# Performance work log

Hardware: AMD Instinct MI355X
Metric: run time of the kernel (lower is better)

## Reference

```python
import jax, jax.numpy as jnp
import numpy as np

N = 16384        # nodes
E = 262144       # edges (avg degree 16)
MUL = 64         # multiplicity per irrep
RDIM = 8         # radial embedding dim
NEURONS = 64     # radial MLP hidden width
NSPECIES = 4
AVG_NEIGH = 16.0
SQRT3 = 1.7320508075688772


def setup_inputs() -> dict:
    key = jax.random.key(0)
    k = jax.random.split(key, 16)
    ey1 = jax.random.normal(k[3], (E, 3), jnp.float32)
    ey1 = ey1 / jnp.linalg.norm(ey1, axis=-1, keepdims=True)  # l=1 spherical harmonics ~ unit edge vectors
    return {
        'node_x0': jax.random.normal(k[0], (N, MUL), jnp.float32),
        'node_x1': jax.random.normal(k[1], (N, MUL, 3), jnp.float32),
        'edge_y0': jnp.ones((E,), jnp.float32),            # l=0 SH is constant
        'edge_y1': ey1,
        'radial_embedding': jax.random.uniform(k[4], (E, RDIM), jnp.float32),
        'senders': jax.random.randint(k[5], (E,), 0, N, dtype=jnp.int32),
        'receivers': jax.random.randint(k[6], (E,), 0, N, dtype=jnp.int32),
        'node_species': jax.random.randint(k[7], (N,), 0, NSPECIES, dtype=jnp.int32),
        'Wup0': jax.random.normal(k[8], (MUL, MUL), jnp.float32),
        'Wup1': jax.random.normal(k[9], (MUL, MUL), jnp.float32),
        'Rw1': jax.random.normal(k[10], (RDIM, NEURONS), jnp.float32),
        'Rw2': jax.random.normal(k[11], (NEURONS, 4 * MUL), jnp.float32),
        'Wd0': jax.random.normal(k[12], (2 * MUL, 2 * MUL), jnp.float32),
        'Wd1': jax.random.normal(k[13], (2 * MUL, MUL), jnp.float32),
        'Wsc0': jax.random.normal(k[14], (NSPECIES, MUL, 2 * MUL), jnp.float32),
        'Wsc1': jax.random.normal(k[15], (NSPECIES, MUL, MUL), jnp.float32),
    }


def reference(node_x0, node_x1, edge_y0, edge_y1, radial_embedding,
              senders, receivers, node_species,
              Wup0, Wup1, Rw1, Rw2, Wd0, Wd1, Wsc0, Wsc1):
    inv = 1.0 / jnp.sqrt(jnp.float32(MUL))
    # ---- linear_up: per-irrep channel mixing --------------------------------
    h0 = (node_x0 @ Wup0) * inv                              # [N, MUL] 0e
    h1 = jnp.einsum('nmc,mk->nkc', node_x1, Wup1) * inv      # [N, MUL, 3] 1o
    # ---- radial MLP -> per-edge tensor-product path weights -----------------
    hid = jax.nn.silu((radial_embedding @ Rw1) / jnp.sqrt(jnp.float32(RDIM)))
    w = ((hid @ Rw2) / jnp.sqrt(jnp.float32(NEURONS))).reshape(E, 4, MUL)
    # ---- gather sender features ---------------------------------------------
    s0 = h0[senders]                                         # [E, MUL]
    s1 = h1[senders]                                         # [E, MUL, 3]
    # ---- CG tensor product (lmax=1) with radial weights ----------------------
    m0a = w[:, 0] * s0 * edge_y0[:, None]                    # 0e x 0e -> 0e
    m0b = w[:, 1] * jnp.einsum('emc,ec->em', s1, edge_y1) / SQRT3  # 1o . 1o -> 0e
    m1a = w[:, 2][:, :, None] * s0[:, :, None] * edge_y1[:, None, :]  # 0e x 1o -> 1o
    m1b = w[:, 3][:, :, None] * s1 * edge_y0[:, None, None]          # 1o x 0e -> 1o
    # ---- scatter-sum to receivers, normalize by sqrt(avg_num_neighbours) ----
    denom = jnp.sqrt(jnp.float32(AVG_NEIGH))
    a0 = jax.ops.segment_sum(jnp.concatenate([m0a, m0b], axis=-1), receivers, num_segments=N) / denom  # [N, 2*MUL]
    a1 = jax.ops.segment_sum(jnp.concatenate([m1a, m1b], axis=1), receivers, num_segments=N) / denom   # [N, 2*MUL, 3]
    # ---- linear_down to gate irreps (MUL scalars + MUL gates, MUL vectors) ---
    inv2 = 1.0 / jnp.sqrt(jnp.float32(2 * MUL))
    d0 = (a0 @ Wd0) * inv2                                   # [N, 2*MUL]
    d1 = jnp.einsum('nmc,mk->nkc', a1, Wd1) * inv2           # [N, MUL, 3]
    # ---- species-indexed self connection (gather weights by species) --------
    all0 = jnp.einsum('nm,smk->nsk', node_x0, Wsc0) * inv    # [N, S, 2*MUL]
    sc0 = jnp.take_along_axis(all0, node_species[:, None, None], axis=1)[:, 0]
    all1 = jnp.einsum('nmc,smk->nskc', node_x1, Wsc1) * inv  # [N, S, MUL, 3]
    sc1 = jnp.take_along_axis(all1, node_species[:, None, None, None], axis=1)[:, 0]
    f0 = 0.5 * (d0 + sc0)
    f1 = 0.5 * (d1 + sc1)
    # ---- equivariant gate: even_act on scalars, even_gate_act on gates ------
    scalars = jax.nn.silu(f0[:, :MUL])                       # [N, MUL]
    gates = jax.nn.silu(f0[:, MUL:])                         # [N, MUL]
    vectors = f1 * gates[:, :, None]                         # [N, MUL, 3]
    return scalars, vectors
```

## Files before the change

kernel.cpp:

```cpp
#include <hip/hip_runtime.h>

#define NN 16384
#define NE 262144
#define N64 (NN * 64)

typedef unsigned short u16;
typedef __attribute__((ext_vector_type(8))) short short8;
typedef __attribute__((ext_vector_type(4))) float f32x4;

__device__ __forceinline__ float us2f(u16 u) {
    union { unsigned int i; float f; } v; v.i = ((unsigned int)u) << 16; return v.f;
}
__device__ __forceinline__ u16 f2us(float x) {
    union { float f; unsigned int i; } u; u.f = x;
    unsigned int r = u.i + 0x7FFF + ((u.i >> 16) & 1);
    return (u16)(r >> 16);
}
__device__ __forceinline__ float silu_f(float x) { return x / (1.0f + __expf(-x)); }
__device__ __forceinline__ float ldf(const void* p, long i, int f) {
    return f ? ((const float*)p)[i] : us2f(((const u16*)p)[i]);
}
__device__ __forceinline__ void ld8(const void* p, long v8, int f, float* o) {
    if (f) {
        const f32x4* q = (const f32x4*)p + v8 * 2;
        f32x4 a = q[0], b = q[1];
        o[0] = a[0]; o[1] = a[1]; o[2] = a[2]; o[3] = a[3];
        o[4] = b[0]; o[5] = b[1]; o[6] = b[2]; o[7] = b[3];
    } else {
        short8 s = ((const short8*)p)[v8];
#pragma unroll
        for (int j = 0; j < 8; j++) o[j] = us2f((u16)s[j]);
    }
}
__device__ __forceinline__ void st8(u16* d, const float* o) {
    short8 s;
#pragma unroll
    for (int j = 0; j < 8; j++) s[j] = (short)f2us(o[j]);
    *reinterpret_cast<short8*>(d) = s;
}
__device__ __forceinline__ short8 f32x8_to_bf16(const float* p) {
    f32x4 a = *reinterpret_cast<const f32x4*>(p);
    f32x4 b = *reinterpret_cast<const f32x4*>(p + 4);
    short8 r;
    r[0] = (short)f2us(a[0]); r[1] = (short)f2us(a[1]);
    r[2] = (short)f2us(a[2]); r[3] = (short)f2us(a[3]);
    r[4] = (short)f2us(b[0]); r[5] = (short)f2us(b[1]);
    r[6] = (short)f2us(b[2]); r[7] = (short)f2us(b[3]);
    return r;
}

__global__ void k_sniff(const u16* __restrict__ re, int* __restrict__ flag,
                        int* __restrict__ cnt) {
    int i = blockIdx.x * 256 + threadIdx.x;
    if (i < NN) cnt[i] = 0;
    if (blockIdx.x == 0 && threadIdx.x < 64) {
        int t = threadIdx.x;
        int hit = (re[t] >= 0x4000) ? 1 : 0;
        unsigned long long b = __ballot(hit);
        if (t == 0) *flag = (__popcll(b) >= 4) ? 1 : 0;
    }
}

#define SB0 1048576L
#define SB1 4194304L
#define SB2 4456448L
#define SB3 5242880L
#define SB4 7340032L
#define SB5 7344128L
#define SB6 7348224L
#define SB7 7348736L
#define SB8 7365120L
#define SB9 7381504L
#define SB10 7389696L
#define SB11 7422464L
#define SB12 7438848L

__global__ void k_convert(const void* x0, const void* x1, const void* ey0, const void* ey1,
                          const void* re, const void* Wup0, const void* Wup1, const void* Rw1,
                          const void* Rw2, const void* Wd0, const void* Wd1, const void* Wsc0,
                          const void* Wsc1, const int* __restrict__ flag,
                          const int* __restrict__ recv, int* __restrict__ cnt,
                          u16* c_x0, u16* x1T, u16* c_ey0, u16* c_ey1, u16* c_re,
                          u16* c_Wup0, u16* c_Wup1, u16* c_Rw1, u16* c_Rw2,
                          u16* c_Wd0, u16* c_Wd1, u16* c_Wsc0, u16* c_Wsc1) {
    long i = (long)blockIdx.x * 256 + threadIdx.x;
    int f = *flag;
    if (i < NE) atomicAdd(&cnt[recv[i]], 1);
    if (i < 131072) {
        float o[8]; ld8(x0, i, f, o); st8(c_x0 + i * 8, o);
    } else if (i < 262144) {
        long v = i - 131072;
        int n = (int)(v >> 3), k8 = (int)(v & 7);
        long b8 = (long)n * 24 + (long)k8 * 3;
        float o[24];
        ld8(x1, b8, f, o); ld8(x1, b8 + 1, f, o + 8); ld8(x1, b8 + 2, f, o + 16);
#pragma unroll
        for (int c = 0; c < 3; c++) {
            float t[8];
#pragma unroll
            for (int k = 0; k < 8; k++) t[k] = o[k * 3 + c];
            st8(x1T + (long)c * N64 + (long)n * 64 + k8 * 8, t);
        }
    } else if (i < 294912) {
        long v = i - 262144; float o[8]; ld8(ey0, v, f, o); st8(c_ey0 + v * 8, o);
    } else if (i < 393216) {
        long v = i - 294912; float o[8]; ld8(ey1, v, f, o); st8(c_ey1 + v * 8, o);
    } else if (i < 655360) {
        long v = i - 393216; float o[8]; ld8(re, v, f, o); st8(c_re + v * 8, o);
    } else {
        long t = i - 655360;
        if (t < 4096)       { long r = t >> 6, c = t & 63;
                              c_Wup0[c * 64 + r] = f2us(ldf(Wup0, t, f)); }
        else if (t < 8192)  { t -= 4096; long r = t >> 6, c = t & 63;
                              c_Wup1[c * 64 + r] = f2us(ldf(Wup1, t, f)); }
        else if (t < 8704)  { t -= 8192; c_Rw1[t] = f2us(ldf(Rw1, t, f)); }
        else if (t < 25088) { t -= 8704; long r = t >> 8, c = t & 255;
                              c_Rw2[c * 64 + r] = f2us(ldf(Rw2, t, f)); }
        else if (t < 41472) { t -= 25088; long r = t >> 7, c = t & 127;
                              c_Wd0[c * 128 + r] = f2us(ldf(Wd0, t, f)); }
        else if (t < 49664) { t -= 41472; long r = t >> 6, c = t & 63;
                              c_Wd1[c * 128 + r] = f2us(ldf(Wd1, t, f)); }
        else if (t < 82432) { t -= 49664; long s = t >> 13, rm = t & 8191;
                              long r = rm >> 7, c = rm & 127;
                              c_Wsc0[s * 8192 + c * 64 + r] = f2us(ldf(Wsc0, t, f)); }
        else                { t -= 82432; long s = t >> 12, rm = t & 4095;
                              long r = rm >> 6, c = rm & 63;
                              c_Wsc1[s * 4096 + c * 64 + r] = f2us(ldf(Wsc1, t, f)); }
    }
}

__global__ void k_scan(const int* __restrict__ cnt, int* __restrict__ offs,
                       int* __restrict__ cursor) {
    __shared__ int sd[256];
    int t = threadIdx.x;
    int base = t * 64;
    const int4* c4 = (const int4*)cnt;
    int loc[64];
#pragma unroll
    for (int i = 0; i < 16; i++) {
        int4 v = c4[t * 16 + i];
        loc[i * 4 + 0] = v.x; loc[i * 4 + 1] = v.y; loc[i * 4 + 2] = v.z; loc[i * 4 + 3] = v.w;
    }
    int sum = 0;
#pragma unroll
    for (int i = 0; i < 64; i++) sum += loc[i];
    sd[t] = sum; __syncthreads();
    for (int off = 1; off < 256; off <<= 1) {
        int v = (t >= off) ? sd[t - off] : 0;
        __syncthreads();
        sd[t] += v;
        __syncthreads();
    }
    int run = sd[t] - sum;
    for (int i = 0; i < 64; i++) {
        offs[base + i] = run; cursor[base + i] = run;
        run += loc[i];
    }
    if (t == 255) offs[NN] = run;
}

__global__ void k_scatter(const int* __restrict__ recv, const int* __restrict__ senders,
                          const u16* __restrict__ ey0, const u16* __restrict__ ey1,
                          int* __restrict__ cursor, int4* __restrict__ meta) {
    int e = blockIdx.x * 256 + threadIdx.x;
    int node = recv[e];
    int p = atomicAdd(&cursor[node], 1);
    unsigned y0  = ey0[e];
    unsigned y1x = ey1[(long)e * 3 + 0];
    unsigned y1y = ey1[(long)e * 3 + 1];
    unsigned y1z = ey1[(long)e * 3 + 2];
    int4 m;
    m.x = senders[e];
    m.y = (int)(y0 | (y1x << 16));
    m.z = (int)(y1y | (y1z << 16));
    m.w = (int)((unsigned)e | ((unsigned)node << 18));
    meta[p] = m;
}

__global__ void k_up_gemm(const u16* __restrict__ x0, const u16* __restrict__ x1T,
                          const u16* __restrict__ Wup0, const u16* __restrict__ Wup1,
                          u16* __restrict__ h) {
    int inst = blockIdx.y;
    int wv = threadIdx.x >> 6, lane = threadIdx.x & 63;
    int lhi = lane >> 4, llo = lane & 15;
    int mb = blockIdx.x * 256 + wv * 64;
    const u16* B = (inst == 0) ? Wup0 : Wup1;
    const u16* A = (inst == 0) ? x0 : (x1T + (long)(inst - 1) * N64);

    short8 bfr[4][2];
#pragma unroll
    for (int t = 0; t < 4; t++)
#pragma unroll
        for (int s = 0; s < 2; s++)
            bfr[t][s] = *reinterpret_cast<const short8*>(B + (long)(t * 16 + llo) * 64 + s * 32 + lhi * 8);

    f32x4 acc[4][4];
#pragma unroll
    for (int i = 0; i < 4; i++)
#pragma unroll
        for (int t = 0; t < 4; t++) acc[i][t] = 0.0f;

#pragma unroll
    for (int s = 0; s < 2; s++) {
        short8 af[4];
#pragma unroll
        for (int i = 0; i < 4; i++)
            af[i] = *reinterpret_cast<const short8*>(A + (long)(mb + i * 16 + llo) * 64 + s * 32 + lhi * 8);
#pragma unroll
        for (int i = 0; i < 4; i++)
#pragma unroll
            for (int t = 0; t < 4; t++)
                acc[i][t] = __builtin_amdgcn_mfma_f32_16x16x32_bf16(af[i], bfr[t][s], acc[i][t], 0, 0, 0);
    }
#pragma unroll
    for (int i = 0; i < 4; i++)
#pragma unroll
        for (int t = 0; t < 4; t++)
#pragma unroll
            for (int r = 0; r < 4; r++)
                h[(long)(mb + i * 16 + lhi * 4 + r) * 256 + (t * 16 + llo) * 4 + inst] =
                    f2us(acc[i][t][r] * 0.125f);
}

#define RROW 268
__global__ void __launch_bounds__(256, 4)
k_edge(const u16* __restrict__ re, const u16* __restrict__ Rw1,
       const u16* __restrict__ Rw2, const int4* __restrict__ meta,
       const u16* __restrict__ h, float* __restrict__ abuf32) {
    __shared__ u16 w_lds[64 * RROW];
    __shared__ int4 meta_s[64];
    u16 (*hid_s)[72] = reinterpret_cast<u16 (*)[72]>(w_lds);

    int tid = threadIdx.x;
    int wv = tid >> 6, lane = tid & 63, lhi = lane >> 4, llo = lane & 15;
    int bid = blockIdx.x;
    int nchunk = gridDim.x >> 3;
    int cblk = (bid & 7) * nchunk + (bid >> 3);
    int p0 = cblk * 64;

    if (tid < 64) meta_s[tid] = meta[p0 + tid];
    __syncthreads();

    {
        int el = tid >> 2;
        int jb = (tid & 3) * 16;
        int e = meta_s[el].w & 0x3FFFF;
        short8 r8 = *reinterpret_cast<const short8*>(re + (long)e * 8);
        float rr[8];
#pragma unroll
        for (int r = 0; r < 8; r++) rr[r] = us2f((u16)r8[r]);
        float hv[16];
#pragma unroll
        for (int q = 0; q < 2; q++) {
            short8 w8 = *reinterpret_cast<const short8*>(Rw1 + jb + q * 8);
#pragma unroll
            for (int j = 0; j < 8; j++) hv[q * 8 + j] = rr[0] * us2f((u16)w8[j]);
        }
#pragma unroll
        for (int r = 1; r < 8; r++) {
#pragma unroll
            for (int q = 0; q < 2; q++) {
                short8 w8 = *reinterpret_cast<const short8*>(Rw1 + (long)r * 64 + jb + q * 8);
#pragma unroll
                for (int j = 0; j < 8; j++) hv[q * 8 + j] += rr[r] * us2f((u16)w8[j]);
            }
        }
#pragma unroll
        for (int q = 0; q < 4; q++) {
            ushort4 pk;
            pk.x = f2us(silu_f(hv[q * 4 + 0] * 0.35355339059327373f));
            pk.y = f2us(silu_f(hv[q * 4 + 1] * 0.35355339059327373f));
            pk.z = f2us(silu_f(hv[q * 4 + 2] * 0.35355339059327373f));
            pk.w = f2us(silu_f(hv[q * 4 + 3] * 0.35355339059327373f));
            *reinterpret_cast<ushort4*>(&hid_s[el][jb + q * 4]) = pk;
        }
    }
    __syncthreads();

    {
        short8 bfr[4][2];
#pragma unroll
        for (int t = 0; t < 4; t++)
#pragma unroll
            for (int s = 0; s < 2; s++)
                bfr[t][s] = *reinterpret_cast<const short8*>(
                    Rw2 + (long)(wv * 64 + t * 16 + llo) * 64 + s * 32 + lhi * 8);
        f32x4 acc[4][4];
#pragma unroll
        for (int i = 0; i < 4; i++)
#pragma unroll
            for (int t = 0; t < 4; t++) acc[i][t] = 0.0f;
#pragma unroll
        for (int s = 0; s < 2; s++) {
            short8 af[4];
#pragma unroll
            for (int i = 0; i < 4; i++)
                af[i] = *reinterpret_cast<const short8*>(&hid_s[i * 16 + llo][s * 32 + lhi * 8]);
#pragma unroll
            for (int i = 0; i < 4; i++)
#pragma unroll
                for (int t = 0; t < 4; t++)
                    acc[i][t] = __builtin_amdgcn_mfma_f32_16x16x32_bf16(af[i], bfr[t][s], acc[i][t], 0, 0, 0);
        }
        __syncthreads();
#pragma unroll
        for (int i = 0; i < 4; i++)
#pragma unroll
            for (int t = 0; t < 4; t++)
#pragma unroll
                for (int r = 0; r < 4; r++)
                    w_lds[(i * 16 + lhi * 4 + r) * RROW + wv * 64 + t * 16 + llo] =
                        f2us(acc[i][t][r] * 0.125f);
    }
    __syncthreads();

    {
        const float qn = 0.25f;
        const float rs3 = 0.57735026918962576f;
        int l = lane;
        int base = wv * 16;

        ushort4 hreg[16];
#pragma unroll
        for (int ss = 0; ss < 16; ss++) {
            int sx = meta_s[base + ss].x;
            hreg[ss] = *reinterpret_cast<const ushort4*>(h + (long)sx * 256 + l * 4);
        }

        float acc[8];
#pragma unroll
        for (int r = 0; r < 8; r++) acc[r] = 0.f;
        int cur = -1;

#pragma unroll
        for (int ss = 0; ss < 16; ss++) {
            int4 m = meta_s[base + ss];
            int node = (int)(((unsigned)m.w) >> 18);
            if (node != cur) {
                if (cur >= 0) {
                    float* dst = abuf32 + (long)cur * 512 + l;
                    atomicAdd(dst,        acc[0] * qn);
                    atomicAdd(dst + 64,   acc[1] * qn * rs3);
                    atomicAdd(dst + 128,  acc[2] * qn);
                    atomicAdd(dst + 192,  acc[3] * qn);
                    atomicAdd(dst + 256,  acc[4] * qn);
                    atomicAdd(dst + 320,  acc[5] * qn);
                    atomicAdd(dst + 384,  acc[6] * qn);
                    atomicAdd(dst + 448,  acc[7] * qn);
                }
                cur = node;
#pragma unroll
                for (int r = 0; r < 8; r++) acc[r] = 0.f;
            }
            int sl = base + ss;
            float w0 = us2f(w_lds[sl * RROW + l]);
            float w1 = us2f(w_lds[sl * RROW + 64 + l]);
            float w2 = us2f(w_lds[sl * RROW + 128 + l]);
            float w3 = us2f(w_lds[sl * RROW + 192 + l]);
            float y0  = us2f((u16)((unsigned)m.y & 0xffff));
            float y1x = us2f((u16)((unsigned)m.y >> 16));
            float y1y = us2f((u16)((unsigned)m.z & 0xffff));
            float y1z = us2f((u16)((unsigned)m.z >> 16));
            float s0 = us2f(hreg[ss].x), s1x = us2f(hreg[ss].y);
            float s1y = us2f(hreg[ss].z), s1z = us2f(hreg[ss].w);
            acc[0] += w0 * s0 * y0;
            acc[1] += w1 * (s1x * y1x + s1y * y1y + s1z * y1z);
            acc[2] += w2 * s0 * y1x;  acc[3] += w3 * s1x * y0;
            acc[4] += w2 * s0 * y1y;  acc[5] += w3 * s1y * y0;
            acc[6] += w2 * s0 * y1z;  acc[7] += w3 * s1z * y0;
        }
        {
            float* dst = abuf32 + (long)cur * 512 + l;
            atomicAdd(dst,        acc[0] * qn);
            atomicAdd(dst + 64,   acc[1] * qn * rs3);
            atomicAdd(dst + 128,  acc[2] * qn);
            atomicAdd(dst + 192,  acc[3] * qn);
            atomicAdd(dst + 256,  acc[4] * qn);
            atomicAdd(dst + 320,  acc[5] * qn);
            atomicAdd(dst + 384,  acc[6] * qn);
            atomicAdd(dst + 448,  acc[7] * qn);
        }
    }
}

#define DN 32
__global__ void __launch_bounds__(320, 3)
k_down(const float* __restrict__ abuf32, const u16* __restrict__ x0,
       const u16* __restrict__ x1T, const int* __restrict__ species,
       const u16* __restrict__ Wd0T, const u16* __restrict__ Wd1T,
       const u16* __restrict__ Wsc0T, const u16* __restrict__ Wsc1T,
       float* __restrict__ out) {
    __shared__ float gate_s[DN][65];
    __shared__ float vec_s[DN * 192];
    __shared__ int sp_s[DN];
    int tid = threadIdx.x;
    int g = tid >> 6;
    int lane = tid & 63, lhi = lane >> 4, llo = lane & 15;
    int node0 = blockIdx.x * DN;
    if (tid < DN) sp_s[tid] = species[node0 + tid];
    __syncthreads();

    const float* Ad; const u16* BdT; int bcol;
    const u16* As; const u16* BsT; int sstr;
    if (g <= 1) { Ad = abuf32; BdT = Wd0T; bcol = g * 64; As = x0; BsT = Wsc0T; sstr = 8192; }
    else        { Ad = abuf32 + (g - 1) * 128; BdT = Wd1T; bcol = 0;
                  As = x1T + (long)(g - 2) * N64; BsT = Wsc1T; sstr = 4096; }

    const float inv2 = 0.08838834764831845f;
    const float inv  = 0.125f;

    short8 a2[DN / 16][2];
#pragma unroll
    for (int rt = 0; rt < DN / 16; rt++)
#pragma unroll
        for (int ks = 0; ks < 2; ks++)
            a2[rt][ks] = *reinterpret_cast<const short8*>(
                As + (long)(node0 + rt * 16 + llo) * 64 + ks * 32 + lhi * 8);

    f32x4 res[DN / 16][4];
#pragma unroll
    for (int rt = 0; rt < DN / 16; rt++)
#pragma unroll
        for (int ct = 0; ct < 4; ct++) res[rt][ct] = 0.0f;

    for (int s = 0; s < 4; s++) {
        short8 bs[4][2];
#pragma unroll
        for (int ct = 0; ct < 4; ct++)
#pragma unroll
            for (int ks = 0; ks < 2; ks++)
                bs[ct][ks] = *reinterpret_cast<const short8*>(
                    BsT + (long)s * sstr + (long)(bcol + ct * 16 + llo) * 64 + ks * 32 + lhi * 8);
#pragma unroll
        for (int rt = 0; rt < DN / 16; rt++) {
            f32x4 accs[4];
#pragma unroll
            for (int ct = 0; ct < 4; ct++) accs[ct] = 0.0f;
#pragma unroll
            for (int ks = 0; ks < 2; ks++)
#pragma unroll
                for (int ct = 0; ct < 4; ct++)
                    accs[ct] = __builtin_amdgcn_mfma_f32_16x16x32_bf16(a2[rt][ks], bs[ct][ks], accs[ct], 0, 0, 0);
#pragma unroll
            for (int r = 0; r < 4; r++) {
                int sp = sp_s[rt * 16 + lhi * 4 + r];
                if (sp == s)
#pragma unroll
                    for (int ct = 0; ct < 4; ct++) res[rt][ct][r] = accs[ct][r];
            }
        }
    }

    short8 bd[4][4];
#pragma unroll
    for (int ct = 0; ct < 4; ct++)
#pragma unroll
        for (int ks = 0; ks < 4; ks++)
            bd[ct][ks] = *reinterpret_cast<const short8*>(
                BdT + (long)(bcol + ct * 16 + llo) * 128 + ks * 32 + lhi * 8);

#pragma unroll
    for (int rt = 0; rt < DN / 16; rt++) {
        f32x4 accd[4];
#pragma unroll
        for (int ct = 0; ct < 4; ct++) accd[ct] = 0.0f;
#pragma unroll
        for (int ks = 0; ks < 4; ks++) {
            short8 a = f32x8_to_bf16(Ad + (long)(node0 + rt * 16 + llo) * 512 + ks * 32 + lhi * 8);
#pragma unroll
            for (int ct = 0; ct < 4; ct++)
                accd[ct] = __builtin_amdgcn_mfma_f32_16x16x32_bf16(a, bd[ct][ks], accd[ct], 0, 0, 0);
        }
#pragma unroll
        for (int ct = 0; ct < 4; ct++)
#pragma unroll
            for (int r = 0; r < 4; r++) {
                float fvv = 0.5f * (accd[ct][r] * inv2 + res[rt][ct][r] * inv);
                int row = rt * 16 + lhi * 4 + r;
                int col = ct * 16 + llo;
                if (g == 0) {
                    out[(long)(node0 + row) * 64 + col] = silu_f(fvv);
                } else if (g == 1) {
                    gate_s[row][col] = silu_f(fvv);
                } else {
                    vec_s[row * 192 + col * 3 + (g - 2)] = fvv;
                }
            }
    }
    __syncthreads();

    {
        float* vout = out + (long)N64 + (long)node0 * 192;
        for (int q4 = tid; q4 < DN * 48; q4 += 320) {
            int q = q4 * 4;
            int row = q4 / 48;
            int rem = q - row * 192;
            f32x4 v = *reinterpret_cast<const f32x4*>(&vec_s[q]);
#pragma unroll
            for (int e = 0; e < 4; e++) v[e] *= gate_s[row][(rem + e) / 3];
            *reinterpret_cast<f32x4*>(vout + q) = v;
        }
    }
}

extern "C" void kernel_launch(void* const* d_in, const int* in_sizes, int n_in,
                              void* d_out, int out_size, void* d_ws, size_t ws_size,
                              hipStream_t stream) {
    const int* senders   = (const int*)d_in[5];
    const int* receivers = (const int*)d_in[6];
    const int* species   = (const int*)d_in[7];
    float* out = (float*)d_out;

    char* ws = (char*)d_ws;
    size_t o = 0;
    auto alloc = [&](size_t bytes) { size_t p = o; o = (o + bytes + 255) & ~255UL; return p; };
    int* flag   = (int*)(ws + alloc(4));
    int* cnt    = (int*)(ws + alloc((size_t)NN * 4));
    int* offs   = (int*)(ws + alloc((size_t)(NN + 1) * 4));
    int* cursor = (int*)(ws + alloc((size_t)NN * 4));
    int4* meta  = (int4*)(ws + alloc((size_t)NE * 16));
    u16* c_x0   = (u16*)(ws + alloc(SB0 * 2));
    u16* x1T    = (u16*)(ws + alloc((size_t)3 * N64 * 2));
    u16* c_ey0  = (u16*)(ws + alloc((SB2 - SB1) * 2));
    u16* c_ey1  = (u16*)(ws + alloc((SB3 - SB2) * 2));
    u16* c_re   = (u16*)(ws + alloc((SB4 - SB3) * 2));
    u16* c_Wup0 = (u16*)(ws + alloc((SB5 - SB4) * 2));
    u16* c_Wup1 = (u16*)(ws + alloc((SB6 - SB5) * 2));
    u16* c_Rw1  = (u16*)(ws + alloc((SB7 - SB6) * 2));
    u16* c_Rw2  = (u16*)(ws + alloc((SB8 - SB7) * 2));
    u16* c_Wd0  = (u16*)(ws + alloc((SB9 - SB8) * 2));
    u16* c_Wd1  = (u16*)(ws + alloc((SB10 - SB9) * 2));
    u16* c_Wsc0 = (u16*)(ws + alloc((SB11 - SB10) * 2));
    u16* c_Wsc1 = (u16*)(ws + alloc((SB12 - SB11) * 2));
    u16* h      = (u16*)(ws + alloc((size_t)NN * 256 * 2));
    float* abuf32 = (float*)(ws + alloc((size_t)NN * 512 * 4));

    k_sniff<<<64, 256, 0, stream>>>((const u16*)d_in[4], flag, cnt);
    (void)hipMemsetAsync(abuf32, 0, (size_t)NN * 512 * 4, stream);
    k_convert<<<2946, 256, 0, stream>>>(d_in[0], d_in[1], d_in[2], d_in[3], d_in[4],
        d_in[8], d_in[9], d_in[10], d_in[11], d_in[12], d_in[13], d_in[14], d_in[15],
        flag, receivers, cnt,
        c_x0, x1T, c_ey0, c_ey1, c_re,
        c_Wup0, c_Wup1, c_Rw1, c_Rw2, c_Wd0, c_Wd1, c_Wsc0, c_Wsc1);
    k_scan<<<1, 256, 0, stream>>>(cnt, offs, cursor);
    k_scatter<<<NE / 256, 256, 0, stream>>>(receivers, senders, c_ey0, c_ey1,
                                            cursor, meta);

    k_up_gemm<<<dim3(NN / 256, 4), 256, 0, stream>>>(c_x0, x1T, c_Wup0, c_Wup1, h);

    k_edge<<<NE / 64, 256, 0, stream>>>(c_re, c_Rw1, c_Rw2, meta, h, abuf32);

    k_down<<<NN / DN, 320, 0, stream>>>(abuf32, c_x0, x1T, species,
                                        c_Wd0, c_Wd1, c_Wsc0, c_Wsc1, out);
}
```

Before: 250.8 us.

## Accumulate edge messages with packed bf16 atomics instead of fp32

The per-node aggregation buffer changes from fp32 to bf16. Edge-kernel scatter now uses packed bf16x2 atomic adds, four per flush instead of eight fp32 atomics, with the channel pairs interleaved. The down-projection weights are permuted to match the interleaved K ordering, and k_down reads bf16 directly instead of converting. This halves the atomic traffic, the memset size and the reads in k_down, but summing in bf16 loses precision across about 16 neighbor contributions and risks exceeding tolerance.

```diff
diff --git a/kernel.cpp b/kernel.cpp
--- a/kernel.cpp
+++ b/kernel.cpp
@@ -1,4 +1,5 @@
 #include <hip/hip_runtime.h>
+#include <hip/hip_bf16.h>
 
 #define NN 16384
 #define NE 262144
@@ -38,15 +39,10 @@
     for (int j = 0; j < 8; j++) s[j] = (short)f2us(o[j]);
     *reinterpret_cast<short8*>(d) = s;
 }
-__device__ __forceinline__ short8 f32x8_to_bf16(const float* p) {
-    f32x4 a = *reinterpret_cast<const f32x4*>(p);
-    f32x4 b = *reinterpret_cast<const f32x4*>(p + 4);
-    short8 r;
-    r[0] = (short)f2us(a[0]); r[1] = (short)f2us(a[1]);
-    r[2] = (short)f2us(a[2]); r[3] = (short)f2us(a[3]);
-    r[4] = (short)f2us(b[0]); r[5] = (short)f2us(b[1]);
-    r[6] = (short)f2us(b[2]); r[7] = (short)f2us(b[3]);
-    return r;
+__device__ __forceinline__ void atom_pk(u16* addr, float a, float b) {
+    unsigned int pk = (unsigned)f2us(a) | ((unsigned)f2us(b) << 16);
+    unsafeAtomicAdd(reinterpret_cast<__hip_bfloat162*>(addr),
+                    *reinterpret_cast<__hip_bfloat162*>(&pk));
 }
 
 __global__ void k_sniff(const u16* __restrict__ re, int* __restrict__ flag,
@@ -117,9 +113,11 @@
         else if (t < 25088) { t -= 8704; long r = t >> 8, c = t & 255;
                               c_Rw2[c * 64 + r] = f2us(ldf(Rw2, t, f)); }
         else if (t < 41472) { t -= 25088; long r = t >> 7, c = t & 127;
-                              c_Wd0[c * 128 + r] = f2us(ldf(Wd0, t, f)); }
+                              long kp = ((r & 63) << 1) | (r >> 6);
+                              c_Wd0[c * 128 + kp] = f2us(ldf(Wd0, t, f)); }
         else if (t < 49664) { t -= 41472; long r = t >> 6, c = t & 63;
-                              c_Wd1[c * 128 + r] = f2us(ldf(Wd1, t, f)); }
+                              long kp = ((r & 63) << 1) | (r >> 6);
+                              c_Wd1[c * 128 + kp] = f2us(ldf(Wd1, t, f)); }
         else if (t < 82432) { t -= 49664; long s = t >> 13, rm = t & 8191;
                               long r = rm >> 7, c = rm & 127;
                               c_Wsc0[s * 8192 + c * 64 + r] = f2us(ldf(Wsc0, t, f)); }
@@ -226,7 +224,7 @@
 __global__ void __launch_bounds__(256, 4)
 k_edge(const u16* __restrict__ re, const u16* __restrict__ Rw1,
        const u16* __restrict__ Rw2, const int4* __restrict__ meta,
-       const u16* __restrict__ h, float* __restrict__ abuf32) {
+       const u16* __restrict__ h, u16* __restrict__ abuf) {
     __shared__ u16 w_lds[64 * RROW];
     __shared__ int4 meta_s[64];
     u16 (*hid_s)[72] = reinterpret_cast<u16 (*)[72]>(w_lds);
@@ -338,15 +336,11 @@
             int node = (int)(((unsigned)m.w) >> 18);
             if (node != cur) {
                 if (cur >= 0) {
-                    float* dst = abuf32 + (long)cur * 512 + l;
-                    atomicAdd(dst,        acc[0] * qn);
-                    atomicAdd(dst + 64,   acc[1] * qn * rs3);
-                    atomicAdd(dst + 128,  acc[2] * qn);
-                    atomicAdd(dst + 192,  acc[3] * qn);
-                    atomicAdd(dst + 256,  acc[4] * qn);
-                    atomicAdd(dst + 320,  acc[5] * qn);
-                    atomicAdd(dst + 384,  acc[6] * qn);
-                    atomicAdd(dst + 448,  acc[7] * qn);
+                    u16* dst = abuf + (long)cur * 512 + l * 2;
+                    atom_pk(dst,       acc[0] * qn, acc[1] * qn * rs3);
+                    atom_pk(dst + 128, acc[2] * qn, acc[3] * qn);
+                    atom_pk(dst + 256, acc[4] * qn, acc[5] * qn);
+                    atom_pk(dst + 384, acc[6] * qn, acc[7] * qn);
                 }
                 cur = node;
 #pragma unroll
@@ -370,22 +364,18 @@
             acc[6] += w2 * s0 * y1z;  acc[7] += w3 * s1z * y0;
         }
         {
-            float* dst = abuf32 + (long)cur * 512 + l;
-            atomicAdd(dst,        acc[0] * qn);
-            atomicAdd(dst + 64,   acc[1] * qn * rs3);
-            atomicAdd(dst + 128,  acc[2] * qn);
-            atomicAdd(dst + 192,  acc[3] * qn);
-            atomicAdd(dst + 256,  acc[4] * qn);
-            atomicAdd(dst + 320,  acc[5] * qn);
-            atomicAdd(dst + 384,  acc[6] * qn);
-            atomicAdd(dst + 448,  acc[7] * qn);
+            u16* dst = abuf + (long)cur * 512 + l * 2;
+            atom_pk(dst,       acc[0] * qn, acc[1] * qn * rs3);
+            atom_pk(dst + 128, acc[2] * qn, acc[3] * qn);
+            atom_pk(dst + 256, acc[4] * qn, acc[5] * qn);
+            atom_pk(dst + 384, acc[6] * qn, acc[7] * qn);
         }
     }
 }
 
 #define DN 32
 __global__ void __launch_bounds__(320, 3)
-k_down(const float* __restrict__ abuf32, const u16* __restrict__ x0,
+k_down(const u16* __restrict__ abuf, const u16* __restrict__ x0,
        const u16* __restrict__ x1T, const int* __restrict__ species,
        const u16* __restrict__ Wd0T, const u16* __restrict__ Wd1T,
        const u16* __restrict__ Wsc0T, const u16* __restrict__ Wsc1T,
@@ -400,10 +390,10 @@
     if (tid < DN) sp_s[tid] = species[node0 + tid];
     __syncthreads();
 
-    const float* Ad; const u16* BdT; int bcol;
+    const u16* Ad; const u16* BdT; int bcol;
     const u16* As; const u16* BsT; int sstr;
-    if (g <= 1) { Ad = abuf32; BdT = Wd0T; bcol = g * 64; As = x0; BsT = Wsc0T; sstr = 8192; }
-    else        { Ad = abuf32 + (g - 1) * 128; BdT = Wd1T; bcol = 0;
+    if (g <= 1) { Ad = abuf; BdT = Wd0T; bcol = g * 64; As = x0; BsT = Wsc0T; sstr = 8192; }
+    else        { Ad = abuf + (g - 1) * 128; BdT = Wd1T; bcol = 0;
                   As = x1T + (long)(g - 2) * N64; BsT = Wsc1T; sstr = 4096; }
 
     const float inv2 = 0.08838834764831845f;
@@ -466,7 +456,8 @@
         for (int ct = 0; ct < 4; ct++) accd[ct] = 0.0f;
 #pragma unroll
         for (int ks = 0; ks < 4; ks++) {
-            short8 a = f32x8_to_bf16(Ad + (long)(node0 + rt * 16 + llo) * 512 + ks * 32 + lhi * 8);
+            short8 a = *reinterpret_cast<const short8*>(
+                Ad + (long)(node0 + rt * 16 + llo) * 512 + ks * 32 + lhi * 8);
 #pragma unroll
             for (int ct = 0; ct < 4; ct++)
                 accd[ct] = __builtin_amdgcn_mfma_f32_16x16x32_bf16(a, bd[ct][ks], accd[ct], 0, 0, 0);
@@ -533,10 +524,10 @@
     u16* c_Wsc0 = (u16*)(ws + alloc((SB11 - SB10) * 2));
     u16* c_Wsc1 = (u16*)(ws + alloc((SB12 - SB11) * 2));
     u16* h      = (u16*)(ws + alloc((size_t)NN * 256 * 2));
-    float* abuf32 = (float*)(ws + alloc((size_t)NN * 512 * 4));
+    u16* abuf   = (u16*)(ws + alloc((size_t)NN * 512 * 2));
 
     k_sniff<<<64, 256, 0, stream>>>((const u16*)d_in[4], flag, cnt);
-    (void)hipMemsetAsync(abuf32, 0, (size_t)NN * 512 * 4, stream);
+    (void)hipMemsetAsync(abuf, 0, (size_t)NN * 512 * 2, stream);
     k_convert<<<2946, 256, 0, stream>>>(d_in[0], d_in[1], d_in[2], d_in[3], d_in[4],
         d_in[8], d_in[9], d_in[10], d_in[11], d_in[12], d_in[13], d_in[14], d_in[15],
         flag, receivers, cnt,
@@ -548,8 +539,8 @@
 
     k_up_gemm<<<dim3(NN / 256, 4), 256, 0, stream>>>(c_x0, x1T, c_Wup0, c_Wup1, h);
 
-    k_edge<<<NE / 64, 256, 0, stream>>>(c_re, c_Rw1, c_Rw2, meta, h, abuf32);
-
-    k_down<<<NN / DN, 320, 0, stream>>>(abuf32, c_x0, x1T, species,
+    k_edge<<<NE / 64, 256, 0, stream>>>(c_re, c_Rw1, c_Rw2, meta, h, abuf);
+
+    k_down<<<NN / DN, 320, 0, stream>>>(abuf, c_x0, x1T, species,
                                         c_Wd0, c_Wd1, c_Wsc0, c_Wsc1, out);
 }
```

Result: faster. 235.9 us (-5.9%).
